# Kernel optimization log

Measured on AMD Instinct MI355X. Metric: run time of the kernel, lower is better.

The kernel has to match this reference:

```python
import jax, jax.numpy as jnp
import numpy as np

COMMITMENT = 1e-4
EPS = 1e-12  # F.normalize eps


def setup_inputs() -> dict:
    key = jax.random.key(0)
    k1, k2 = jax.random.split(key)
    b, h, l, d, c = 4, 8, 4096, 64, 512
    x = jax.random.normal(k1, (b, h, l, d), dtype=jnp.float32)
    means = jax.random.normal(k2, (h, c, d), dtype=jnp.float32)
    return {"x": x, "means": means}


def reference(x, means):
    # x: [b,h,l,d], means: [h,c,d]
    h = means.shape[0]
    # F.normalize(x, 2, dim=-1): x / max(||x||, eps)
    norm = jnp.linalg.norm(x, axis=-1, keepdims=True)
    xn = x / jnp.maximum(norm, EPS)
    # cosine similarity to cluster centers: [b,h,l,c]
    dists = jnp.einsum('bhld,hcd->bhlc', xn, means)
    buckets = jnp.argmax(dists, axis=-1)  # [b,h,l]
    # batched_index_select of means per (head, bucket): [b,h,l,d]
    routed_means = means[jnp.arange(h)[None, :, None], buckets]
    loss = jnp.mean((xn - routed_means) ** 2) * COMMITMENT
    return dists, loss
```

## Files before the change

### kernel.cpp

```cpp
#include <hip/hip_runtime.h>
#include <hip/hip_bf16.h>

#define NB 4
#define NH 8
#define NL 4096
#define ND 64
#define NC 512
#define TILE_L 128
#define NBLOCKS (NB * NH * (NL / TILE_L))
#define EPSV 1e-12f
#define COMMITV 0.0001f

typedef __attribute__((ext_vector_type(8))) short bf16x8;
typedef __attribute__((ext_vector_type(4))) float f32x4;

__device__ __forceinline__ unsigned bfpack(float a, float b) {
    unsigned ua = __float_as_uint(a);
    unsigned ub = __float_as_uint(b);
    ua = (ua + 0x7fffu + ((ua >> 16) & 1u)) >> 16;
    ub = (ub + 0x7fffu + ((ub >> 16) & 1u)) & 0xffff0000u;
    return (ua & 0xffffu) | ub;
}

union bfrag { unsigned u[4]; bf16x8 v; };

__global__ __launch_bounds__(512, 4) void kmeans_kernel(
    const float* __restrict__ x, const float* __restrict__ means,
    float* __restrict__ dists, float* __restrict__ part)
{
    __shared__ alignas(16) unsigned short m_lds[NC * ND];
    __shared__ float msq[NC];
    __shared__ float wsum[8];

    const int t = threadIdx.x;
    const int ltiles = NL / TILE_L;
    const int bh = blockIdx.x / ltiles;
    const int l0 = (blockIdx.x % ltiles) * TILE_L;
    const int h  = bh & (NH - 1);

    const float4* mp = (const float4*)(means + (size_t)h * NC * ND);
    #pragma unroll 4
    for (int i = 0; i < 16; ++i) {
        int f4 = t + i * 512;
        float4 v = mp[f4];
        int row = f4 >> 4;
        int q = f4 & 15;
        float ss = v.x * v.x + v.y * v.y + v.z * v.z + v.w * v.w;
        ss += __shfl_xor(ss, 1); ss += __shfl_xor(ss, 2);
        ss += __shfl_xor(ss, 4); ss += __shfl_xor(ss, 8);
        if ((t & 15) == 0) msq[row] = ss;
        unsigned lo = bfpack(v.x, v.y), hi = bfpack(v.z, v.w);
        int byte = row * 128 + ((q * 8) ^ ((row & 7) << 4));
        *(unsigned long long*)((char*)m_lds + byte) =
            (unsigned long long)lo | ((unsigned long long)hi << 32);
    }

    const int wave = t >> 6, lane = t & 63;
    const int r16 = lane & 15, g = lane >> 4;

    const int xrow = l0 + wave * 16 + r16;
    const float4* xr = (const float4*)(x + ((size_t)bh * NL + xrow) * ND);
    float4 v0 = xr[g * 2], v1 = xr[g * 2 + 1];
    float4 v2 = xr[8 + g * 2], v3 = xr[8 + g * 2 + 1];

    float ss = v0.x*v0.x + v0.y*v0.y + v0.z*v0.z + v0.w*v0.w
             + v1.x*v1.x + v1.y*v1.y + v1.z*v1.z + v1.w*v1.w
             + v2.x*v2.x + v2.y*v2.y + v2.z*v2.z + v2.w*v2.w
             + v3.x*v3.x + v3.y*v3.y + v3.z*v3.z + v3.w*v3.w;
    ss += __shfl_xor(ss, 16);
    ss += __shfl_xor(ss, 32);
    const float inv = 1.0f / fmaxf(sqrtf(ss), EPSV);
    const float sn2 = ss * inv * inv;

    bfrag a0f, a1f;
    a0f.u[0] = bfpack(v0.x * inv, v0.y * inv); a0f.u[1] = bfpack(v0.z * inv, v0.w * inv);
    a0f.u[2] = bfpack(v1.x * inv, v1.y * inv); a0f.u[3] = bfpack(v1.z * inv, v1.w * inv);
    a1f.u[0] = bfpack(v2.x * inv, v2.y * inv); a1f.u[1] = bfpack(v2.z * inv, v2.w * inv);
    a1f.u[2] = bfpack(v3.x * inv, v3.y * inv); a1f.u[3] = bfpack(v3.z * inv, v3.w * inv);
    const bf16x8 a0 = a0f.v, a1 = a1f.v;

    __syncthreads();

    float mx[4]; int mi[4];
    #pragma unroll
    for (int r = 0; r < 4; ++r) { mx[r] = -1e30f; mi[r] = 0; }

    const size_t obase = ((size_t)bh * NL + l0 + wave * 16) * NC;

    #pragma unroll 4
    for (int c0 = 0; c0 < NC; c0 += 16) {
        int brow = c0 + r16;
        const char* mb = (const char*)m_lds + brow * 128;
        const int bsw = (brow & 7) << 4;
        bf16x8 b0 = *(const bf16x8*)(mb + ((g * 16) ^ bsw));
        bf16x8 b1 = *(const bf16x8*)(mb + ((64 + g * 16) ^ bsw));
        f32x4 acc = {0.f, 0.f, 0.f, 0.f};
        acc = __builtin_amdgcn_mfma_f32_16x16x32_bf16(a0, b0, acc, 0, 0, 0);
        acc = __builtin_amdgcn_mfma_f32_16x16x32_bf16(a1, b1, acc, 0, 0, 0);
        #pragma unroll
        for (int r = 0; r < 4; ++r) {
            float v = acc[r];
            __builtin_nontemporal_store(v,
                &dists[obase + (size_t)(g * 4 + r) * NC + (c0 + r16)]);
            if (v > mx[r]) { mx[r] = v; mi[r] = c0 + r16; }
        }
    }

    #pragma unroll
    for (int s = 1; s < 16; s <<= 1) {
        #pragma unroll
        for (int r = 0; r < 4; ++r) {
            float ov = __shfl_xor(mx[r], s);
            int   oi = __shfl_xor(mi[r], s);
            if (ov > mx[r] || (ov == mx[r] && oi < mi[r])) { mx[r] = ov; mi[r] = oi; }
        }
    }

    float sacc = 0.f;
    #pragma unroll
    for (int r = 0; r < 4; ++r) {
        float s2 = __shfl(sn2, g * 4 + r);
        sacc += s2 - 2.f * mx[r] + msq[mi[r]];
    }
    if (r16 != 0) sacc = 0.f;
    sacc += __shfl_xor(sacc, 16);
    sacc += __shfl_xor(sacc, 32);
    if (lane == 0) wsum[wave] = sacc;
    __syncthreads();
    if (t == 0) {
        float s = 0.f;
        #pragma unroll
        for (int w = 0; w < 8; ++w) s += wsum[w];
        part[blockIdx.x] = s;
    }
}

__global__ __launch_bounds__(256) void loss_reduce(
    const float* __restrict__ part, float* __restrict__ loss)
{
    __shared__ float w[4];
    const int t = threadIdx.x;
    float s = 0.f;
    #pragma unroll
    for (int i = 0; i < NBLOCKS / 256; ++i) s += part[t + i * 256];
    s += __shfl_xor(s, 1);  s += __shfl_xor(s, 2);  s += __shfl_xor(s, 4);
    s += __shfl_xor(s, 8);  s += __shfl_xor(s, 16); s += __shfl_xor(s, 32);
    if ((t & 63) == 0) w[t >> 6] = s;
    __syncthreads();
    if (t == 0)
        loss[0] = (w[0] + w[1] + w[2] + w[3]) *
                  (COMMITV / (float)((size_t)NB * NH * NL * ND));
}

extern "C" void kernel_launch(void* const* d_in, const int* in_sizes, int n_in,
                              void* d_out, int out_size, void* d_ws, size_t ws_size,
                              hipStream_t stream) {
    const float* x = (const float*)d_in[0];
    const float* means = (const float*)d_in[1];
    float* dists = (float*)d_out;
    float* loss = dists + (size_t)NB * NH * NL * NC;
    float* part = (float*)d_ws;

    kmeans_kernel<<<dim3(NBLOCKS), dim3(512), 0, stream>>>(x, means, dists, part);
    loss_reduce<<<dim3(1), dim3(256), 0, stream>>>(part, loss);
}
```

Baseline: 330.2 us.

## Switch to 32x32x16 MFMA tiles with 256-row L tiles per block

Replaces the 16x16x32 bf16 MFMA scheme with 32x32x16 MFMAs, so each wave computes a 32-row by 32-centroid output tile per step. The L tile per block doubles to 256 rows, which halves the block count and halves how often the full means table is reloaded and converted into LDS. The A fragments, the output row mapping, the argmax shuffle reduction and the loss accumulation are all rewritten for the 32-lane layout. The kernel is bound by writing the dists output, so the gain depends on whether larger tiles cut setup cost. The cost is more accumulator and argmax registers per thread and fewer blocks, which may reduce occupancy.

```diff
diff --git a/kernel.cpp b/kernel.cpp
--- a/kernel.cpp
+++ b/kernel.cpp
@@ -6,13 +6,13 @@
 #define NL 4096
 #define ND 64
 #define NC 512
-#define TILE_L 128
+#define TILE_L 256
 #define NBLOCKS (NB * NH * (NL / TILE_L))
 #define EPSV 1e-12f
 #define COMMITV 0.0001f
 
 typedef __attribute__((ext_vector_type(8))) short bf16x8;
-typedef __attribute__((ext_vector_type(4))) float f32x4;
+typedef __attribute__((ext_vector_type(16))) float f32x16;
 
 __device__ __forceinline__ unsigned bfpack(float a, float b) {
     unsigned ua = __float_as_uint(a);
@@ -49,67 +49,81 @@
         ss += __shfl_xor(ss, 1); ss += __shfl_xor(ss, 2);
         ss += __shfl_xor(ss, 4); ss += __shfl_xor(ss, 8);
         if ((t & 15) == 0) msq[row] = ss;
-        unsigned lo = bfpack(v.x, v.y), hi = bfpack(v.z, v.w);
+        unsigned lo = bfpack(v.x, v.y), hi2 = bfpack(v.z, v.w);
         int byte = row * 128 + ((q * 8) ^ ((row & 7) << 4));
         *(unsigned long long*)((char*)m_lds + byte) =
-            (unsigned long long)lo | ((unsigned long long)hi << 32);
+            (unsigned long long)lo | ((unsigned long long)hi2 << 32);
     }
 
     const int wave = t >> 6, lane = t & 63;
-    const int r16 = lane & 15, g = lane >> 4;
+    const int l31 = lane & 31, hi = lane >> 5;
 
-    const int xrow = l0 + wave * 16 + r16;
+    const int xrow = l0 + wave * 32 + l31;
     const float4* xr = (const float4*)(x + ((size_t)bh * NL + xrow) * ND);
-    float4 v0 = xr[g * 2], v1 = xr[g * 2 + 1];
-    float4 v2 = xr[8 + g * 2], v3 = xr[8 + g * 2 + 1];
-
-    float ss = v0.x*v0.x + v0.y*v0.y + v0.z*v0.z + v0.w*v0.w
-             + v1.x*v1.x + v1.y*v1.y + v1.z*v1.z + v1.w*v1.w
-             + v2.x*v2.x + v2.y*v2.y + v2.z*v2.z + v2.w*v2.w
-             + v3.x*v3.x + v3.y*v3.y + v3.z*v3.z + v3.w*v3.w;
-    ss += __shfl_xor(ss, 16);
+    float4 xv[8];
+    #pragma unroll
+    for (int kk = 0; kk < 4; ++kk) {
+        xv[2 * kk]     = xr[4 * kk + 2 * hi];
+        xv[2 * kk + 1] = xr[4 * kk + 2 * hi + 1];
+    }
+    float ss = 0.f;
+    #pragma unroll
+    for (int i = 0; i < 8; ++i)
+        ss += xv[i].x * xv[i].x + xv[i].y * xv[i].y
+            + xv[i].z * xv[i].z + xv[i].w * xv[i].w;
     ss += __shfl_xor(ss, 32);
     const float inv = 1.0f / fmaxf(sqrtf(ss), EPSV);
     const float sn2 = ss * inv * inv;
 
-    bfrag a0f, a1f;
-    a0f.u[0] = bfpack(v0.x * inv, v0.y * inv); a0f.u[1] = bfpack(v0.z * inv, v0.w * inv);
-    a0f.u[2] = bfpack(v1.x * inv, v1.y * inv); a0f.u[3] = bfpack(v1.z * inv, v1.w * inv);
-    a1f.u[0] = bfpack(v2.x * inv, v2.y * inv); a1f.u[1] = bfpack(v2.z * inv, v2.w * inv);
-    a1f.u[2] = bfpack(v3.x * inv, v3.y * inv); a1f.u[3] = bfpack(v3.z * inv, v3.w * inv);
-    const bf16x8 a0 = a0f.v, a1 = a1f.v;
+    bfrag a0, a1, a2, a3;
+    #pragma unroll
+    for (int j = 0; j < 2; ++j) {
+        a0.u[2*j] = bfpack(xv[j].x * inv, xv[j].y * inv);
+        a0.u[2*j+1] = bfpack(xv[j].z * inv, xv[j].w * inv);
+        a1.u[2*j] = bfpack(xv[2+j].x * inv, xv[2+j].y * inv);
+        a1.u[2*j+1] = bfpack(xv[2+j].z * inv, xv[2+j].w * inv);
+        a2.u[2*j] = bfpack(xv[4+j].x * inv, xv[4+j].y * inv);
+        a2.u[2*j+1] = bfpack(xv[4+j].z * inv, xv[4+j].w * inv);
+        a3.u[2*j] = bfpack(xv[6+j].x * inv, xv[6+j].y * inv);
+        a3.u[2*j+1] = bfpack(xv[6+j].z * inv, xv[6+j].w * inv);
+    }
+    const bf16x8 af0 = a0.v, af1 = a1.v, af2 = a2.v, af3 = a3.v;
 
     __syncthreads();
 
-    float mx[4]; int mi[4];
+    float mx[16]; int mi[16];
     #pragma unroll
-    for (int r = 0; r < 4; ++r) { mx[r] = -1e30f; mi[r] = 0; }
+    for (int r = 0; r < 16; ++r) { mx[r] = -1e30f; mi[r] = 0; }
 
-    const size_t obase = ((size_t)bh * NL + l0 + wave * 16) * NC;
+    const size_t obase = ((size_t)bh * NL + l0 + wave * 32) * NC;
 
-    #pragma unroll 4
-    for (int c0 = 0; c0 < NC; c0 += 16) {
-        int brow = c0 + r16;
+    for (int c0 = 0; c0 < NC; c0 += 32) {
+        int brow = c0 + l31;
         const char* mb = (const char*)m_lds + brow * 128;
         const int bsw = (brow & 7) << 4;
-        bf16x8 b0 = *(const bf16x8*)(mb + ((g * 16) ^ bsw));
-        bf16x8 b1 = *(const bf16x8*)(mb + ((64 + g * 16) ^ bsw));
-        f32x4 acc = {0.f, 0.f, 0.f, 0.f};
-        acc = __builtin_amdgcn_mfma_f32_16x16x32_bf16(a0, b0, acc, 0, 0, 0);
-        acc = __builtin_amdgcn_mfma_f32_16x16x32_bf16(a1, b1, acc, 0, 0, 0);
+        bf16x8 b0 = *(const bf16x8*)(mb + ((0  + 16 * hi) ^ bsw));
+        bf16x8 b1 = *(const bf16x8*)(mb + ((32 + 16 * hi) ^ bsw));
+        bf16x8 b2 = *(const bf16x8*)(mb + ((64 + 16 * hi) ^ bsw));
+        bf16x8 b3 = *(const bf16x8*)(mb + ((96 + 16 * hi) ^ bsw));
+        f32x16 acc = {};
+        acc = __builtin_amdgcn_mfma_f32_32x32x16_bf16(af0, b0, acc, 0, 0, 0);
+        acc = __builtin_amdgcn_mfma_f32_32x32x16_bf16(af1, b1, acc, 0, 0, 0);
+        acc = __builtin_amdgcn_mfma_f32_32x32x16_bf16(af2, b2, acc, 0, 0, 0);
+        acc = __builtin_amdgcn_mfma_f32_32x32x16_bf16(af3, b3, acc, 0, 0, 0);
         #pragma unroll
-        for (int r = 0; r < 4; ++r) {
+        for (int r = 0; r < 16; ++r) {
             float v = acc[r];
+            int row = (r & 3) + 8 * (r >> 2) + 4 * hi;
             __builtin_nontemporal_store(v,
-                &dists[obase + (size_t)(g * 4 + r) * NC + (c0 + r16)]);
-            if (v > mx[r]) { mx[r] = v; mi[r] = c0 + r16; }
+                &dists[obase + (size_t)row * NC + (c0 + l31)]);
+            if (v > mx[r]) { mx[r] = v; mi[r] = c0 + l31; }
         }
     }
 
     #pragma unroll
-    for (int s = 1; s < 16; s <<= 1) {
+    for (int s = 1; s < 32; s <<= 1) {
         #pragma unroll
-        for (int r = 0; r < 4; ++r) {
+        for (int r = 0; r < 16; ++r) {
             float ov = __shfl_xor(mx[r], s);
             int   oi = __shfl_xor(mi[r], s);
             if (ov > mx[r] || (ov == mx[r] && oi < mi[r])) { mx[r] = ov; mi[r] = oi; }
@@ -118,12 +132,12 @@
 
     float sacc = 0.f;
     #pragma unroll
-    for (int r = 0; r < 4; ++r) {
-        float s2 = __shfl(sn2, g * 4 + r);
+    for (int r = 0; r < 16; ++r) {
+        int rl = (r & 3) + 8 * (r >> 2) + 4 * hi;
+        float s2 = __shfl(sn2, rl);
         sacc += s2 - 2.f * mx[r] + msq[mi[r]];
     }
-    if (r16 != 0) sacc = 0.f;
-    sacc += __shfl_xor(sacc, 16);
+    if (l31 != 0) sacc = 0.f;
     sacc += __shfl_xor(sacc, 32);
     if (lane == 0) wsum[wave] = sacc;
     __syncthreads();
```

Measured after the change: 312.4 us. -5.4%, faster.
